# Performance work log

Measured on AMD Instinct MI355X. Metric: run time of the kernel, lower is better.

Reference implementation:

```python
import jax, jax.numpy as jnp
import numpy as np

L, H, D, V, TMAX = 12, 12, 768, 50257, 1024
B, T = 2, 1024
HD = D // H
EPS = 1e-5


def new_gelu(x):
    return 0.5 * x * (1.0 + jnp.tanh(jnp.sqrt(2.0 / jnp.pi) * (x + 0.044715 * x ** 3)))


def layer_norm(x, w, b):
    mu = jnp.mean(x, axis=-1, keepdims=True)
    var = jnp.var(x, axis=-1, keepdims=True)
    return (x - mu) * jax.lax.rsqrt(var + EPS) * w + b


def setup_inputs() -> dict:
    key = jax.random.key(0)
    ks = jax.random.split(key, 12)
    s = 0.02
    return {
        "idx": jax.random.randint(ks[0], (B, T), 0, V),
        "wte": jax.random.normal(ks[1], (V, D), jnp.float32) * s,
        "wpe": jax.random.normal(ks[2], (TMAX, D), jnp.float32) * s,
        "ln1_w": jnp.ones((L, D), jnp.float32),
        "ln1_b": jnp.zeros((L, D), jnp.float32),
        "attn_w": jax.random.normal(ks[3], (L, D, 3 * D), jnp.float32) * s,
        "attn_b": jnp.zeros((L, 3 * D), jnp.float32),
        "proj_w": jax.random.normal(ks[4], (L, D, D), jnp.float32) * (s / jnp.sqrt(2.0 * L)),
        "proj_b": jnp.zeros((L, D), jnp.float32),
        "ln2_w": jnp.ones((L, D), jnp.float32),
        "ln2_b": jnp.zeros((L, D), jnp.float32),
        "fc_w": jax.random.normal(ks[5], (L, D, 4 * D), jnp.float32) * s,
        "fc_b": jnp.zeros((L, 4 * D), jnp.float32),
        "fc2_w": jax.random.normal(ks[6], (L, 4 * D, D), jnp.float32) * (s / jnp.sqrt(2.0 * L)),
        "fc2_b": jnp.zeros((L, D), jnp.float32),
        "lnf_w": jnp.ones((D,), jnp.float32),
        "lnf_b": jnp.zeros((D,), jnp.float32),
        "lm_head_w": jax.random.normal(ks[7], (D, V), jnp.float32) * s,
    }


def _gpt_forward(idx, wte, wpe, ln1_w, ln1_b, attn_w, attn_b, proj_w, proj_b,
                 ln2_w, ln2_b, fc_w, fc_b, fc2_w, fc2_b, lnf_w, lnf_b, lm_head_w):
    b, t = idx.shape
    x = wte[idx] + wpe[:t][None, :, :]  # [B,T,D]
    causal = jnp.tril(jnp.ones((t, t), bool))  # [T,T]
    scale = 1.0 / jnp.sqrt(jnp.asarray(HD, x.dtype))

    layer_params = {
        "ln1_w": ln1_w, "ln1_b": ln1_b, "attn_w": attn_w, "attn_b": attn_b,
        "proj_w": proj_w, "proj_b": proj_b, "ln2_w": ln2_w, "ln2_b": ln2_b,
        "fc_w": fc_w, "fc_b": fc_b, "fc2_w": fc2_w, "fc2_b": fc2_b,
    }

    def block(x, p):
        h = layer_norm(x, p["ln1_w"], p["ln1_b"])
        qkv = h @ p["attn_w"] + p["attn_b"]  # [B,T,3D]
        q, k, v = jnp.split(qkv, 3, axis=-1)
        q = q.reshape(b, t, H, HD)
        k = k.reshape(b, t, H, HD)
        v = v.reshape(b, t, H, HD)
        att = jnp.einsum("bqhd,bkhd->bhqk", q, k) * scale
        att = jnp.where(causal[None, None, :, :], att, -jnp.inf)
        att = jax.nn.softmax(att, axis=-1)
        y = jnp.einsum("bhqk,bkhd->bqhd", att, v).reshape(b, t, D)
        x = x + y @ p["proj_w"] + p["proj_b"]
        h2 = layer_norm(x, p["ln2_w"], p["ln2_b"])
        m = new_gelu(h2 @ p["fc_w"] + p["fc_b"])
        x = x + m @ p["fc2_w"] + p["fc2_b"]
        return x, None

    x, _ = jax.lax.scan(block, x, layer_params)
    x = layer_norm(x, lnf_w, lnf_b)
    logits = x @ lm_head_w  # [B,T,V]
    return logits


def reference(idx, wte, wpe, ln1_w, ln1_b, attn_w, attn_b, proj_w, proj_b,
              ln2_w, ln2_b, fc_w, fc_b, fc2_w, fc2_b, lnf_w, lnf_b, lm_head_w):
    return _gpt_forward(idx, wte, wpe, ln1_w, ln1_b, attn_w, attn_b, proj_w, proj_b,
                        ln2_w, ln2_b, fc_w, fc_b, fc2_w, fc2_b, lnf_w, lnf_b, lm_head_w)
```

## Files before the change

kernel.cpp:

```cpp
#include <hip/hip_runtime.h>
#include <math.h>

#define Bsz  2
#define Tlen 1024
#define Dm   768
#define Hh   12
#define HDm  64
#define Ll   12
#define Vv   50257
#define Mrows (Bsz * Tlen)

typedef __attribute__((ext_vector_type(8))) short short8;
typedef __attribute__((ext_vector_type(4))) float f32x4;

__device__ __forceinline__ float bf2f(unsigned short u) {
  union { unsigned int i; float f; } v; v.i = ((unsigned int)u) << 16; return v.f;
}
__device__ __forceinline__ unsigned short f2bf(float f) {
  union { float f; unsigned int i; } v; v.f = f;
  unsigned int u = v.i;
  return (unsigned short)((u + 0x7FFFu + ((u >> 16) & 1u)) >> 16);
}
__device__ __forceinline__ float gelu_f(float x) {
  const float c = 0.7978845608028654f;
  return 0.5f * x * (1.0f + tanhf(c * (x + 0.044715f * x * x * x)));
}

__device__ __forceinline__ void gl_lds16(const unsigned short* g, unsigned short* l) {
  __builtin_amdgcn_global_load_lds(
      (const __attribute__((address_space(1))) unsigned int*)g,
      (__attribute__((address_space(3))) unsigned int*)l, 16, 0, 0);
}

__global__ void embed_kernel(const int* __restrict__ idx, const float* __restrict__ wte,
                             const float* __restrict__ wpe, float* __restrict__ x) {
  int i = (blockIdx.x * 256 + threadIdx.x) * 4;
  int d = i % Dm;
  int bt = i / Dm;
  int t = bt % Tlen;
  int tok = idx[bt];
  float4 a = *(const float4*)(wte + (size_t)tok * Dm + d);
  float4 p = *(const float4*)(wpe + (size_t)t * Dm + d);
  float4 r; r.x = a.x + p.x; r.y = a.y + p.y; r.z = a.z + p.z; r.w = a.w + p.w;
  *(float4*)(x + i) = r;
}

__global__ __launch_bounds__(256) void ln_wave(const float* __restrict__ x,
                                               const float* __restrict__ w,
                                               const float* __restrict__ b,
                                               unsigned short* __restrict__ out) {
  int tid = threadIdx.x, wv = tid >> 6, l = tid & 63;
  int row = blockIdx.x * 4 + wv;
  const float* xr = x + (size_t)row * Dm;
  float4 v[3];
  float s = 0.f, s2 = 0.f;
#pragma unroll
  for (int i = 0; i < 3; ++i) {
    v[i] = *(const float4*)(xr + l * 4 + i * 256);
    s += v[i].x + v[i].y + v[i].z + v[i].w;
    s2 += v[i].x * v[i].x + v[i].y * v[i].y + v[i].z * v[i].z + v[i].w * v[i].w;
  }
#pragma unroll
  for (int o = 1; o < 64; o <<= 1) {
    s += __shfl_xor(s, o, 64);
    s2 += __shfl_xor(s2, o, 64);
  }
  float mu = s * (1.0f / Dm);
  float var = s2 * (1.0f / Dm) - mu * mu;
  float rstd = rsqrtf(var + 1e-5f);
  unsigned short* yr = out + (size_t)row * Dm;
#pragma unroll
  for (int i = 0; i < 3; ++i) {
    float4 wv4 = *(const float4*)(w + l * 4 + i * 256);
    float4 bv4 = *(const float4*)(b + l * 4 + i * 256);
    ushort4 o4;
    o4.x = f2bf((v[i].x - mu) * rstd * wv4.x + bv4.x);
    o4.y = f2bf((v[i].y - mu) * rstd * wv4.y + bv4.y);
    o4.z = f2bf((v[i].z - mu) * rstd * wv4.z + bv4.z);
    o4.w = f2bf((v[i].w - mu) * rstd * wv4.w + bv4.w);
    *(ushort4*)(yr + l * 4 + i * 256) = o4;
  }
}

__global__ __launch_bounds__(256) void tconv_kernel(const float* __restrict__ W, int ldw,
                                                    int nValid, unsigned short* __restrict__ WT,
                                                    int K) {
  __shared__ float S[32][33];
  int n0 = blockIdx.x * 32, k0 = blockIdx.y * 32;
  int t = threadIdx.x;
  int nc = t & 31, kr0 = t >> 5;
#pragma unroll
  for (int i = 0; i < 4; ++i) {
    int kr = kr0 + i * 8;
    S[kr][nc] = (n0 + nc < nValid) ? W[(size_t)(k0 + kr) * ldw + n0 + nc] : 0.f;
  }
  __syncthreads();
  int r = t >> 3, c4 = (t & 7) * 4;
  ushort4 o;
  o.x = f2bf(S[c4 + 0][r]); o.y = f2bf(S[c4 + 1][r]);
  o.z = f2bf(S[c4 + 2][r]); o.w = f2bf(S[c4 + 3][r]);
  *(ushort4*)(WT + (size_t)(n0 + r) * K + k0 + c4) = o;
}

__global__ __launch_bounds__(256) void tconv4_kernel(
    const float* __restrict__ wA, const float* __restrict__ wP,
    const float* __restrict__ wF, const float* __restrict__ wF2,
    unsigned short* __restrict__ oA, unsigned short* __restrict__ oP,
    unsigned short* __restrict__ oF, unsigned short* __restrict__ oF2) {
  int bid = blockIdx.x;
  const float* W; unsigned short* WT; int ldw, K, ntn, local;
  if (bid < 1728)      { W = wA;  WT = oA;  ldw = 2304; K = 768;  ntn = 72; local = bid; }
  else if (bid < 2304) { W = wP;  WT = oP;  ldw = 768;  K = 768;  ntn = 24; local = bid - 1728; }
  else if (bid < 4608) { W = wF;  WT = oF;  ldw = 3072; K = 768;  ntn = 96; local = bid - 2304; }
  else                 { W = wF2; WT = oF2; ldw = 768;  K = 3072; ntn = 24; local = bid - 4608; }
  int n0 = (local % ntn) * 32, k0 = (local / ntn) * 32;
  __shared__ float S[32][33];
  int t = threadIdx.x;
  int nc = t & 31, kr0 = t >> 5;
#pragma unroll
  for (int i = 0; i < 4; ++i) {
    int kr = kr0 + i * 8;
    S[kr][nc] = W[(size_t)(k0 + kr) * ldw + n0 + nc];
  }
  __syncthreads();
  int r = t >> 3, c4 = (t & 7) * 4;
  ushort4 o;
  o.x = f2bf(S[c4 + 0][r]); o.y = f2bf(S[c4 + 1][r]);
  o.z = f2bf(S[c4 + 2][r]); o.w = f2bf(S[c4 + 3][r]);
  *(ushort4*)(WT + (size_t)(n0 + r) * K + k0 + c4) = o;
}

__global__ __launch_bounds__(256) void gemm_bf16(
    const unsigned short* __restrict__ A, const unsigned short* __restrict__ B, int K,
    const float* __restrict__ bias, const float* __restrict__ res,
    float* __restrict__ outF, unsigned short* __restrict__ outB,
    int ldc, int nValid, int act) {
  __shared__ alignas(16) unsigned short As[128][32];
  __shared__ alignas(16) unsigned short Bs[128][32];
  int tid = threadIdx.x;
  int rowBase = blockIdx.y * 128;
  int colBase = blockIdx.x * 128;
  int w = tid >> 6, l = tid & 63;
  int wr = w >> 1, wc = w & 1;

  int srow = tid >> 2;
  int skk = (tid & 3) * 8;
  const unsigned short* aSrc = A + (size_t)(rowBase + srow) * K + skk;
  const unsigned short* bSrc = B + (size_t)(colBase + srow) * K + skk;
  unsigned short* aL0 = &As[w * 16][0];
  unsigned short* aL1 = &As[w * 16 + 64][0];
  unsigned short* bL0 = &Bs[w * 16][0];
  unsigned short* bL1 = &Bs[w * 16 + 64][0];

  f32x4 acc[4][4];
#pragma unroll
  for (int m = 0; m < 4; ++m)
#pragma unroll
    for (int n = 0; n < 4; ++n) acc[m][n] = (f32x4){0.f, 0.f, 0.f, 0.f};

  int fr = l & 15, fq = l >> 4;

  for (int k0 = 0; k0 < K; k0 += 32) {
    gl_lds16(aSrc + k0, aL0);
    gl_lds16(aSrc + (size_t)64 * K + k0, aL1);
    gl_lds16(bSrc + k0, bL0);
    gl_lds16(bSrc + (size_t)64 * K + k0, bL1);
    asm volatile("s_waitcnt vmcnt(0)" ::: "memory");
    __syncthreads();

    short8 af[4], bfr[4];
#pragma unroll
    for (int m = 0; m < 4; ++m)
      af[m] = *(const short8*)&As[wr * 64 + m * 16 + fr][fq * 8];
#pragma unroll
    for (int n = 0; n < 4; ++n)
      bfr[n] = *(const short8*)&Bs[wc * 64 + n * 16 + fr][fq * 8];
#pragma unroll
    for (int m = 0; m < 4; ++m)
#pragma unroll
      for (int n = 0; n < 4; ++n)
        acc[m][n] = __builtin_amdgcn_mfma_f32_16x16x32_bf16(af[m], bfr[n], acc[m][n], 0, 0, 0);
    __syncthreads();
  }

#pragma unroll
  for (int m = 0; m < 4; ++m) {
    int row = rowBase + wr * 64 + m * 16 + fq * 4;
#pragma unroll
    for (int n = 0; n < 4; ++n) {
      int col = colBase + wc * 64 + n * 16 + fr;
      if (col >= nValid) continue;
      float bv = bias ? bias[col] : 0.f;
#pragma unroll
      for (int j = 0; j < 4; ++j) {
        float v = acc[m][n][j] + bv;
        if (act) v = gelu_f(v);
        if (res) v += res[(size_t)(row + j) * ldc + col];
        if (outF) outF[(size_t)(row + j) * ldc + col] = v;
        else      outB[(size_t)(row + j) * ldc + col] = f2bf(v);
      }
    }
  }
}

__global__ __launch_bounds__(256) void gemm_bf16_sm(
    const unsigned short* __restrict__ A, const unsigned short* __restrict__ B, int K,
    const float* __restrict__ bias, const float* __restrict__ res,
    float* __restrict__ outF, unsigned short* __restrict__ outB,
    int ldc, int act) {
  __shared__ alignas(16) unsigned short As[64][32];
  __shared__ alignas(16) unsigned short Bs[128][32];
  int tid = threadIdx.x;
  int rowBase = blockIdx.y * 64;
  int colBase = blockIdx.x * 128;
  int w = tid >> 6, l = tid & 63;
  int fr = l & 15, fq = l >> 4;

  int srow = l >> 2, skk = (l & 3) * 8;
  const unsigned short* aSrc = A + (size_t)(rowBase + w * 16 + srow) * K + skk;
  const unsigned short* bSrc = B + (size_t)(colBase + w * 16 + srow) * K + skk;
  unsigned short* aL = &As[w * 16][0];
  unsigned short* bL0 = &Bs[w * 16][0];
  unsigned short* bL1 = &Bs[w * 16 + 64][0];

  f32x4 acc[4][2];
#pragma unroll
  for (int m = 0; m < 4; ++m)
#pragma unroll
    for (int n = 0; n < 2; ++n) acc[m][n] = (f32x4){0.f, 0.f, 0.f, 0.f};

  for (int k0 = 0; k0 < K; k0 += 32) {
    gl_lds16(aSrc + k0, aL);
    gl_lds16(bSrc + k0, bL0);
    gl_lds16(bSrc + (size_t)64 * K + k0, bL1);
    asm volatile("s_waitcnt vmcnt(0)" ::: "memory");
    __syncthreads();

    short8 af[4], bfr[2];
#pragma unroll
    for (int m = 0; m < 4; ++m)
      af[m] = *(const short8*)&As[m * 16 + fr][fq * 8];
#pragma unroll
    for (int n = 0; n < 2; ++n)
      bfr[n] = *(const short8*)&Bs[w * 32 + n * 16 + fr][fq * 8];
#pragma unroll
    for (int m = 0; m < 4; ++m)
#pragma unroll
      for (int n = 0; n < 2; ++n)
        acc[m][n] = __builtin_amdgcn_mfma_f32_16x16x32_bf16(af[m], bfr[n], acc[m][n], 0, 0, 0);
    __syncthreads();
  }

#pragma unroll
  for (int m = 0; m < 4; ++m) {
    int row = rowBase + m * 16 + fq * 4;
#pragma unroll
    for (int n = 0; n < 2; ++n) {
      int col = colBase + w * 32 + n * 16 + fr;
      float bv = bias ? bias[col] : 0.f;
#pragma unroll
      for (int j = 0; j < 4; ++j) {
        float v = acc[m][n][j] + bv;
        if (act) v = gelu_f(v);
        if (res) v += res[(size_t)(row + j) * ldc + col];
        if (outF) outF[(size_t)(row + j) * ldc + col] = v;
        else      outB[(size_t)(row + j) * ldc + col] = f2bf(v);
      }
    }
  }
}

__global__ __launch_bounds__(256) void attn_mfma(const unsigned short* __restrict__ qkv,
                                                 unsigned short* __restrict__ y) {
  int bx = blockIdx.x;
  int qt = bx & 15;
  int h  = (bx >> 4) % Hh;
  int b  = bx / (16 * Hh);
  int q0 = qt * 64;
  int tid = threadIdx.x;
  int w = tid >> 6, l = tid & 63;
  int g = l >> 4, fr = l & 15;

  __shared__ alignas(16) unsigned short Kl[2][4096];
  __shared__ alignas(16) unsigned short Vt[4096];
  __shared__ alignas(16) unsigned short Pl[4][1024];

  const size_t rs = 3 * Dm;
  const unsigned short* base = qkv + (size_t)(b * Tlen) * rs + h * HDm;

  short8 qf[2];
  {
    const unsigned short* qrow = base + (size_t)(q0 + w * 16 + fr) * rs;
    qf[0] = *(const short8*)(qrow + g * 8);
    qf[1] = *(const short8*)(qrow + g * 8 + 32);
  }

  int vt_t = tid >> 2, vt_dc = tid & 3;
  uint4 v0r, v1r;

  f32x4 oAcc[4];
#pragma unroll
  for (int nd = 0; nd < 4; ++nd) oAcc[nd] = (f32x4){0.f, 0.f, 0.f, 0.f};
  float mRun[4] = {-1e30f, -1e30f, -1e30f, -1e30f};
  float lRun[4] = {0.f, 0.f, 0.f, 0.f};

  unsigned short* Pw = &Pl[w][0];
  int nkt = qt + 1;

  {
#pragma unroll
    for (int i = 0; i < 2; ++i) {
      int c = i * 256 + tid;
      int t = c >> 3, cl = c & 7;
      int dch = cl ^ (t & 7);
      gl_lds16(base + (size_t)t * rs + Dm + dch * 8, &Kl[0][(i * 256 + w * 64) * 8]);
    }
    const unsigned short* p = base + (size_t)vt_t * rs + 2 * Dm + vt_dc * 16;
    v0r = *(const uint4*)p;
    v1r = *(const uint4*)(p + 8);
  }

  for (int kt = 0; kt < nkt; ++kt) {
    int cur = kt & 1;
    int kbase = kt * 64;
    asm volatile("s_waitcnt vmcnt(0)" ::: "memory");
    __builtin_amdgcn_s_barrier();

    {
      union { uint4 u; unsigned short s[8]; } a, bb;
      a.u = v0r; bb.u = v1r;
#pragma unroll
      for (int j = 0; j < 8; ++j) {
        int d = vt_dc * 16 + j;
        Vt[d * 64 + (vt_t ^ ((d & 7) << 3))] = a.s[j];
        int d2 = d + 8;
        Vt[d2 * 64 + (vt_t ^ ((d2 & 7) << 3))] = bb.s[j];
      }
    }
    if (kt + 1 < nkt) {
      int kb = kbase + 64;
#pragma unroll
      for (int i = 0; i < 2; ++i) {
        int c = i * 256 + tid;
        int t = c >> 3, cl = c & 7;
        int dch = cl ^ (t & 7);
        gl_lds16(base + (size_t)(kb + t) * rs + Dm + dch * 8,
                 &Kl[cur ^ 1][(i * 256 + w * 64) * 8]);
      }
      const unsigned short* p = base + (size_t)(kb + vt_t) * rs + 2 * Dm + vt_dc * 16;
      v0r = *(const uint4*)p;
      v1r = *(const uint4*)(p + 8);
    }
    asm volatile("s_waitcnt lgkmcnt(0)" ::: "memory");
    __builtin_amdgcn_s_barrier();

    f32x4 sAcc[4];
#pragma unroll
    for (int nt = 0; nt < 4; ++nt) sAcc[nt] = (f32x4){0.f, 0.f, 0.f, 0.f};
#pragma unroll
    for (int ks = 0; ks < 2; ++ks)
#pragma unroll
      for (int nt = 0; nt < 4; ++nt) {
        int kcol = nt * 16 + fr;
        short8 kf = *(const short8*)&Kl[cur][kcol * 64 + ((g * 8 + ks * 32) ^ ((kcol & 7) << 3))];
        sAcc[nt] = __builtin_amdgcn_mfma_f32_16x16x32_bf16(qf[ks], kf, sAcc[nt], 0, 0, 0);
      }

    float corr[4];
#pragma unroll
    for (int j = 0; j < 4; ++j) {
      int qg = q0 + w * 16 + g * 4 + j;
      float tm = -1e30f;
#pragma unroll
      for (int nt = 0; nt < 4; ++nt) {
        float s = sAcc[nt][j] * 0.125f;
        int tg = kbase + nt * 16 + fr;
        if (tg > qg) s = -1e30f;
        sAcc[nt][j] = s;
        tm = fmaxf(tm, s);
      }
      tm = fmaxf(tm, __shfl_xor(tm, 1, 16));
      tm = fmaxf(tm, __shfl_xor(tm, 2, 16));
      tm = fmaxf(tm, __shfl_xor(tm, 4, 16));
      tm = fmaxf(tm, __shfl_xor(tm, 8, 16));
      float mN = fmaxf(mRun[j], tm);
      corr[j] = __expf(mRun[j] - mN);
      mRun[j] = mN;
      float ps = 0.f;
#pragma unroll
      for (int nt = 0; nt < 4; ++nt) {
        float p = __expf(sAcc[nt][j] - mN);
        sAcc[nt][j] = p;
        ps += p;
      }
      ps += __shfl_xor(ps, 1, 16);
      ps += __shfl_xor(ps, 2, 16);
      ps += __shfl_xor(ps, 4, 16);
      ps += __shfl_xor(ps, 8, 16);
      lRun[j] = lRun[j] * corr[j] + ps;
    }

#pragma unroll
    for (int nt = 0; nt < 4; ++nt)
#pragma unroll
      for (int j = 0; j < 4; ++j) {
        int q = g * 4 + j;
        int t = nt * 16 + fr;
        Pw[q * 64 + (t ^ ((q & 7) << 3))] = f2bf(sAcc[nt][j]);
      }
#pragma unroll
    for (int nd = 0; nd < 4; ++nd)
#pragma unroll
      for (int j = 0; j < 4; ++j) oAcc[nd][j] *= corr[j];

#pragma unroll
    for (int ks = 0; ks < 2; ++ks) {
      short8 pf = *(const short8*)&Pw[fr * 64 + ((g * 8 + ks * 32) ^ ((fr & 7) << 3))];
#pragma unroll
      for (int nd = 0; nd < 4; ++nd) {
        int d = nd * 16 + fr;
        short8 vf = *(const short8*)&Vt[d * 64 + ((g * 8 + ks * 32) ^ ((fr & 7) << 3))];
        oAcc[nd] = __builtin_amdgcn_mfma_f32_16x16x32_bf16(pf, vf, oAcc[nd], 0, 0, 0);
      }
    }
  }

#pragma unroll
  for (int j = 0; j < 4; ++j) {
    float inv = 1.0f / lRun[j];
    int q = q0 + w * 16 + g * 4 + j;
    unsigned short* yr = y + (size_t)(b * Tlen + q) * Dm + h * HDm + fr;
#pragma unroll
    for (int nd = 0; nd < 4; ++nd)
      yr[nd * 16] = f2bf(oAcc[nd][j] * inv);
  }
}

extern "C" void kernel_launch(void* const* d_in, const int* in_sizes, int n_in,
                              void* d_out, int out_size, void* d_ws, size_t ws_size,
                              hipStream_t stream) {
  const int*   idx    = (const int*)d_in[0];
  const float* wte    = (const float*)d_in[1];
  const float* wpe    = (const float*)d_in[2];
  const float* ln1_w  = (const float*)d_in[3];
  const float* ln1_b  = (const float*)d_in[4];
  const float* attn_w = (const float*)d_in[5];
  const float* attn_b = (const float*)d_in[6];
  const float* proj_w = (const float*)d_in[7];
  const float* proj_b = (const float*)d_in[8];
  const float* ln2_w  = (const float*)d_in[9];
  const float* ln2_b  = (const float*)d_in[10];
  const float* fc_w   = (const float*)d_in[11];
  const float* fc_b   = (const float*)d_in[12];
  const float* fc2_w  = (const float*)d_in[13];
  const float* fc2_b  = (const float*)d_in[14];
  const float* lnf_w  = (const float*)d_in[15];
  const float* lnf_b  = (const float*)d_in[16];
  const float* lmw    = (const float*)d_in[17];
  float* out = (float*)d_out;

  float* x = (float*)d_ws;
  unsigned short* qkvb = (unsigned short*)(x + (size_t)Mrows * Dm);
  unsigned short* xb   = qkvb + (size_t)Mrows * 3 * Dm;
  unsigned short* yb   = xb + (size_t)Mrows * Dm;
  unsigned short* mb   = yb + (size_t)Mrows * Dm;
  unsigned short* wbuf = mb + (size_t)Mrows * 4 * Dm;
  unsigned short* wAttn = wbuf;
  unsigned short* wProj = wAttn + (size_t)3 * Dm * Dm;
  unsigned short* wFc   = wProj + (size_t)Dm * Dm;
  unsigned short* wFc2  = wFc + (size_t)4 * Dm * Dm;

  const size_t baseBytes = (size_t)Mrows * Dm * 4 + (size_t)Mrows * 9 * Dm * 2;
  size_t availShorts = (ws_size - baseBytes) / 2;
  long long cc = (long long)(availShorts / Dm) & ~127LL;
  if (cc > 50304) cc = 50304;
  const int chunkCols = (int)cc;

  embed_kernel<<<(Mrows * Dm) / 1024, 256, 0, stream>>>(idx, wte, wpe, x);

  for (int l = 0; l < Ll; ++l) {
    tconv4_kernel<<<6912, 256, 0, stream>>>(
        attn_w + (size_t)l * Dm * 3 * Dm, proj_w + (size_t)l * Dm * Dm,
        fc_w + (size_t)l * Dm * 4 * Dm, fc2_w + (size_t)l * 4 * Dm * Dm,
        wAttn, wProj, wFc, wFc2);

    ln_wave<<<Mrows / 4, 256, 0, stream>>>(x, ln1_w + l * Dm, ln1_b + l * Dm, xb);
    gemm_bf16_sm<<<dim3(18, 32), 256, 0, stream>>>(xb, wAttn, Dm, attn_b + (size_t)l * 3 * Dm,
                                                   nullptr, nullptr, qkvb, 3 * Dm, 0);
    attn_mfma<<<Bsz * Hh * 16, 256, 0, stream>>>(qkvb, yb);
    gemm_bf16_sm<<<dim3(6, 32), 256, 0, stream>>>(yb, wProj, Dm, proj_b + (size_t)l * Dm,
                                                  x, x, nullptr, Dm, 0);
    ln_wave<<<Mrows / 4, 256, 0, stream>>>(x, ln2_w + l * Dm, ln2_b + l * Dm, xb);
    gemm_bf16_sm<<<dim3(24, 32), 256, 0, stream>>>(xb, wFc, Dm, fc_b + (size_t)l * 4 * Dm,
                                                   nullptr, nullptr, mb, 4 * Dm, 1);
    gemm_bf16_sm<<<dim3(6, 32), 256, 0, stream>>>(mb, wFc2, 4 * Dm, fc2_b + (size_t)l * Dm,
                                                  x, x, nullptr, Dm, 0);
  }

  ln_wave<<<Mrows / 4, 256, 0, stream>>>(x, lnf_w, lnf_b, xb);
  for (int base = 0; base < Vv; base += chunkCols) {
    int ncv = Vv - base; if (ncv > chunkCols) ncv = chunkCols;
    int ntiles = (ncv + 127) / 128;
    tconv_kernel<<<dim3((ncv + 31) / 32, 24), 256, 0, stream>>>(lmw + base, Vv, ncv, wbuf, Dm);
    gemm_bf16<<<dim3(ntiles, 16), 256, 0, stream>>>(xb, wbuf, Dm, nullptr, nullptr,
                                                    out + base, nullptr, Vv, ncv, 0);
  }
}
```

Baseline: 2.667 ms.

## Double-buffer LDS in GEMMs, swap lm_head grid order, use nontemporal stores

Both bf16 GEMM kernels now keep two LDS buffers and prefetch the next K-slice with partial vmcnt waits, so global loads overlap the MFMA work instead of stalling every iteration. The lm_head GEMM is templated so its grid puts row tiles on x, which makes consecutive blocks share the same weight column tile. Its fp32 logits are written with nontemporal stores to avoid polluting cache. The cost is doubled LDS use, which may lower occupancy, and the raw s_barrier calls depend on the waitcnt ordering being correct.

```diff
diff --git a/kernel.cpp b/kernel.cpp
--- a/kernel.cpp
+++ b/kernel.cpp
@@ -130,27 +130,23 @@
   *(ushort4*)(WT + (size_t)(n0 + r) * K + k0 + c4) = o;
 }
 
-__global__ __launch_bounds__(256) void gemm_bf16(
+template<bool SWAPGRID, bool NTSTORE>
+__global__ __launch_bounds__(256) void gemm_big(
     const unsigned short* __restrict__ A, const unsigned short* __restrict__ B, int K,
     const float* __restrict__ bias, const float* __restrict__ res,
     float* __restrict__ outF, unsigned short* __restrict__ outB,
     int ldc, int nValid, int act) {
-  __shared__ alignas(16) unsigned short As[128][32];
-  __shared__ alignas(16) unsigned short Bs[128][32];
+  __shared__ alignas(16) unsigned short As[2][128][32];
+  __shared__ alignas(16) unsigned short Bs[2][128][32];
   int tid = threadIdx.x;
-  int rowBase = blockIdx.y * 128;
-  int colBase = blockIdx.x * 128;
+  int bcol = SWAPGRID ? (int)blockIdx.y : (int)blockIdx.x;
+  int brow = SWAPGRID ? (int)blockIdx.x : (int)blockIdx.y;
+  int rowBase = brow * 128, colBase = bcol * 128;
   int w = tid >> 6, l = tid & 63;
   int wr = w >> 1, wc = w & 1;
-
-  int srow = tid >> 2;
-  int skk = (tid & 3) * 8;
+  int srow = tid >> 2, skk = (tid & 3) * 8;
   const unsigned short* aSrc = A + (size_t)(rowBase + srow) * K + skk;
   const unsigned short* bSrc = B + (size_t)(colBase + srow) * K + skk;
-  unsigned short* aL0 = &As[w * 16][0];
-  unsigned short* aL1 = &As[w * 16 + 64][0];
-  unsigned short* bL0 = &Bs[w * 16][0];
-  unsigned short* bL1 = &Bs[w * 16 + 64][0];
 
   f32x4 acc[4][4];
 #pragma unroll
@@ -160,27 +156,40 @@
 
   int fr = l & 15, fq = l >> 4;
 
-  for (int k0 = 0; k0 < K; k0 += 32) {
-    gl_lds16(aSrc + k0, aL0);
-    gl_lds16(aSrc + (size_t)64 * K + k0, aL1);
-    gl_lds16(bSrc + k0, bL0);
-    gl_lds16(bSrc + (size_t)64 * K + k0, bL1);
-    asm volatile("s_waitcnt vmcnt(0)" ::: "memory");
-    __syncthreads();
+  gl_lds16(aSrc, &As[0][w * 16][0]);
+  gl_lds16(aSrc + (size_t)64 * K, &As[0][w * 16 + 64][0]);
+  gl_lds16(bSrc, &Bs[0][w * 16][0]);
+  gl_lds16(bSrc + (size_t)64 * K, &Bs[0][w * 16 + 64][0]);
+
+  int nIt = K >> 5;
+  for (int it = 0; it < nIt; ++it) {
+    int cur = it & 1;
+    int k0 = it * 32;
+    if (it + 1 < nIt) {
+      int nx = cur ^ 1;
+      gl_lds16(aSrc + k0 + 32, &As[nx][w * 16][0]);
+      gl_lds16(aSrc + (size_t)64 * K + k0 + 32, &As[nx][w * 16 + 64][0]);
+      gl_lds16(bSrc + k0 + 32, &Bs[nx][w * 16][0]);
+      gl_lds16(bSrc + (size_t)64 * K + k0 + 32, &Bs[nx][w * 16 + 64][0]);
+      asm volatile("s_waitcnt vmcnt(4)" ::: "memory");
+    } else {
+      asm volatile("s_waitcnt vmcnt(0)" ::: "memory");
+    }
+    asm volatile("s_barrier" ::: "memory");
 
     short8 af[4], bfr[4];
 #pragma unroll
     for (int m = 0; m < 4; ++m)
-      af[m] = *(const short8*)&As[wr * 64 + m * 16 + fr][fq * 8];
+      af[m] = *(const short8*)&As[cur][wr * 64 + m * 16 + fr][fq * 8];
 #pragma unroll
     for (int n = 0; n < 4; ++n)
-      bfr[n] = *(const short8*)&Bs[wc * 64 + n * 16 + fr][fq * 8];
+      bfr[n] = *(const short8*)&Bs[cur][wc * 64 + n * 16 + fr][fq * 8];
 #pragma unroll
     for (int m = 0; m < 4; ++m)
 #pragma unroll
       for (int n = 0; n < 4; ++n)
         acc[m][n] = __builtin_amdgcn_mfma_f32_16x16x32_bf16(af[m], bfr[n], acc[m][n], 0, 0, 0);
-    __syncthreads();
+    asm volatile("s_barrier" ::: "memory");
   }
 
 #pragma unroll
@@ -196,8 +205,12 @@
         float v = acc[m][n][j] + bv;
         if (act) v = gelu_f(v);
         if (res) v += res[(size_t)(row + j) * ldc + col];
-        if (outF) outF[(size_t)(row + j) * ldc + col] = v;
-        else      outB[(size_t)(row + j) * ldc + col] = f2bf(v);
+        if (outF) {
+          if (NTSTORE) __builtin_nontemporal_store(v, &outF[(size_t)(row + j) * ldc + col]);
+          else outF[(size_t)(row + j) * ldc + col] = v;
+        } else {
+          outB[(size_t)(row + j) * ldc + col] = f2bf(v);
+        }
       }
     }
   }
@@ -208,8 +221,8 @@
     const float* __restrict__ bias, const float* __restrict__ res,
     float* __restrict__ outF, unsigned short* __restrict__ outB,
     int ldc, int act) {
-  __shared__ alignas(16) unsigned short As[64][32];
-  __shared__ alignas(16) unsigned short Bs[128][32];
+  __shared__ alignas(16) unsigned short As[2][64][32];
+  __shared__ alignas(16) unsigned short Bs[2][128][32];
   int tid = threadIdx.x;
   int rowBase = blockIdx.y * 64;
   int colBase = blockIdx.x * 128;
@@ -219,9 +232,6 @@
   int srow = l >> 2, skk = (l & 3) * 8;
   const unsigned short* aSrc = A + (size_t)(rowBase + w * 16 + srow) * K + skk;
   const unsigned short* bSrc = B + (size_t)(colBase + w * 16 + srow) * K + skk;
-  unsigned short* aL = &As[w * 16][0];
-  unsigned short* bL0 = &Bs[w * 16][0];
-  unsigned short* bL1 = &Bs[w * 16 + 64][0];
 
   f32x4 acc[4][2];
 #pragma unroll
@@ -229,26 +239,38 @@
 #pragma unroll
     for (int n = 0; n < 2; ++n) acc[m][n] = (f32x4){0.f, 0.f, 0.f, 0.f};
 
-  for (int k0 = 0; k0 < K; k0 += 32) {
-    gl_lds16(aSrc + k0, aL);
-    gl_lds16(bSrc + k0, bL0);
-    gl_lds16(bSrc + (size_t)64 * K + k0, bL1);
-    asm volatile("s_waitcnt vmcnt(0)" ::: "memory");
-    __syncthreads();
+  gl_lds16(aSrc, &As[0][w * 16][0]);
+  gl_lds16(bSrc, &Bs[0][w * 16][0]);
+  gl_lds16(bSrc + (size_t)64 * K, &Bs[0][w * 16 + 64][0]);
+
+  int nIt = K >> 5;
+  for (int it = 0; it < nIt; ++it) {
+    int cur = it & 1;
+    int k0 = it * 32;
+    if (it + 1 < nIt) {
+      int nx = cur ^ 1;
+      gl_lds16(aSrc + k0 + 32, &As[nx][w * 16][0]);
+      gl_lds16(bSrc + k0 + 32, &Bs[nx][w * 16][0]);
+      gl_lds16(bSrc + (size_t)64 * K + k0 + 32, &Bs[nx][w * 16 + 64][0]);
+      asm volatile("s_waitcnt vmcnt(3)" ::: "memory");
+    } else {
+      asm volatile("s_waitcnt vmcnt(0)" ::: "memory");
+    }
+    asm volatile("s_barrier" ::: "memory");
 
     short8 af[4], bfr[2];
 #pragma unroll
     for (int m = 0; m < 4; ++m)
-      af[m] = *(const short8*)&As[m * 16 + fr][fq * 8];
+      af[m] = *(const short8*)&As[cur][m * 16 + fr][fq * 8];
 #pragma unroll
     for (int n = 0; n < 2; ++n)
-      bfr[n] = *(const short8*)&Bs[w * 32 + n * 16 + fr][fq * 8];
+      bfr[n] = *(const short8*)&Bs[cur][w * 32 + n * 16 + fr][fq * 8];
 #pragma unroll
     for (int m = 0; m < 4; ++m)
 #pragma unroll
       for (int n = 0; n < 2; ++n)
         acc[m][n] = __builtin_amdgcn_mfma_f32_16x16x32_bf16(af[m], bfr[n], acc[m][n], 0, 0, 0);
-    __syncthreads();
+    asm volatile("s_barrier" ::: "memory");
   }
 
 #pragma unroll
@@ -502,7 +524,7 @@
     int ncv = Vv - base; if (ncv > chunkCols) ncv = chunkCols;
     int ntiles = (ncv + 127) / 128;
     tconv_kernel<<<dim3((ncv + 31) / 32, 24), 256, 0, stream>>>(lmw + base, Vv, ncv, wbuf, Dm);
-    gemm_bf16<<<dim3(ntiles, 16), 256, 0, stream>>>(xb, wbuf, Dm, nullptr, nullptr,
-                                                    out + base, nullptr, Vv, ncv, 0);
-  }
-}
+    gemm_big<true, true><<<dim3(16, ntiles), 256, 0, stream>>>(
+        xb, wbuf, Dm, nullptr, nullptr, out + base, nullptr, Vv, ncv, 0);
+  }
+}
```

Result: slower. 2.772 ms (+3.9%).
